# Performance work log

Measured on AMD Instinct MI355X. Metric: run time of the kernel, lower is better.

## Reference

```python
import jax, jax.numpy as jnp
import numpy as np

V, S, D, H, L, F = 32000, 1024, 1024, 16, 6, 4096
DH = D // H          # 64
HALF = DH // 2       # 32
EPS = 1e-5
ROPE_BASE = 10000.0


def setup_inputs() -> dict:
    key = jax.random.key(0)
    ks = jax.random.split(key, 16)
    std = 0.02
    inp = {
        "tokens": jax.random.randint(ks[0], (4, S), 0, V),
        "tok_emb": jax.random.normal(ks[1], (V, D), jnp.float32) * std,
        "ln1_s": jnp.ones((L, D), jnp.float32),
        "ln1_b": jnp.zeros((L, D), jnp.float32),
        "w_qkv": jax.random.normal(ks[2], (L, D, 3 * D), jnp.float32) * std,
        "w_proj": jax.random.normal(ks[3], (L, D, D), jnp.float32) * std,
        "ln2_s": jnp.ones((L, D), jnp.float32),
        "ln2_b": jnp.zeros((L, D), jnp.float32),
        "w_in": jax.random.normal(ks[4], (L, D, 2 * F), jnp.float32) * std,
        "w_out": jax.random.normal(ks[5], (L, F, D), jnp.float32) * std,
        "lnf_s": jnp.ones((D,), jnp.float32),
        "lnf_b": jnp.zeros((D,), jnp.float32),
        "w_score": jax.random.normal(ks[6], (D, 1), jnp.float32) * std,
        "w_cls": jax.random.normal(ks[7], (D, S), jnp.float32) * std,
    }
    return inp


def _layernorm(x, s, b):
    m = x.mean(-1, keepdims=True)
    v = ((x - m) ** 2).mean(-1, keepdims=True)
    return (x - m) * jax.lax.rsqrt(v + EPS) * s + b


def _rotate_half(x):
    x_even = x[..., ::2]
    x_odd = x[..., 1::2]
    return jnp.stack((-x_odd, x_even), axis=-1).reshape(x.shape)


def _rope_tables():
    inv_freq = 1.0 / (ROPE_BASE ** (jnp.arange(0, DH, 2, dtype=jnp.float32) / DH))
    pos = jnp.arange(S, dtype=jnp.float32)
    freqs = jnp.outer(pos, inv_freq)               # [S, DH/2]
    cos = jnp.repeat(jnp.cos(freqs), 2, axis=-1)   # [S, DH]
    sin = jnp.repeat(jnp.sin(freqs), 2, axis=-1)
    return cos, sin


def _forward(tokens, tok_emb, ln1_s, ln1_b, w_qkv, w_proj, ln2_s, ln2_b,
             w_in, w_out, lnf_s, lnf_b, w_score, w_cls):
    B = tokens.shape[0]
    cos, sin = _rope_tables()                      # [S, DH], broadcast over B,H
    lower = jnp.tril(jnp.ones((S, S), jnp.bool_))  # j <= i -> "down" subspace
    scale = HALF ** -0.5

    h = tok_emb[tokens]                            # [B, S, D]

    def block(h, p):
        l1s, l1b, Wqkv, Wp, l2s, l2b, Wi, Wo = p
        # --- dual-triangle attention ---
        qkv = _layernorm(h, l1s, l1b) @ Wqkv       # [B, S, 3D]
        q, k, v = jnp.split(qkv, 3, axis=-1)
        def heads(t):
            return t.reshape(B, S, H, DH).transpose(0, 2, 1, 3)  # [B,H,S,DH]
        q, k, v = heads(q), heads(k), heads(v)
        q = q * cos + _rotate_half(q) * sin
        k = k * cos + _rotate_half(k) * sin
        a_up = jnp.einsum('bhqd,bhkd->bhqk', q[..., :HALF], k[..., :HALF]) * scale
        a_dn = jnp.einsum('bhqd,bhkd->bhqk', q[..., HALF:], k[..., HALF:]) * scale
        logits = jnp.where(lower, a_dn, a_up)
        w = jax.nn.softmax(logits, axis=-1)
        o = jnp.einsum('bhqk,bhkd->bhqd', w, v)
        o = o.transpose(0, 2, 1, 3).reshape(B, S, D) @ Wp
        h = h + o
        # --- SwiGLU MLP ---
        g = _layernorm(h, l2s, l2b) @ Wi           # [B, S, 2F]
        a, b = jnp.split(g, 2, axis=-1)
        h = h + (jax.nn.silu(a) * b) @ Wo
        return h, None

    h, _ = jax.lax.scan(block, h, (ln1_s, ln1_b, w_qkv, w_proj, ln2_s, ln2_b, w_in, w_out))

    # pooling head: per-position scores -> softmax over positions -> weighted sum
    h = _layernorm(h, lnf_s, lnf_b)
    scores = h @ w_score                           # [B, S, 1]
    pw = jax.nn.softmax(scores, axis=1)
    pooled = jnp.sum(pw * h, axis=1)               # [B, D]
    return pooled @ w_cls                          # [B, S] logits over positions


def reference(tokens, tok_emb, ln1_s, ln1_b, w_qkv, w_proj, ln2_s, ln2_b,
              w_in, w_out, lnf_s, lnf_b, w_score, w_cls):
    return _forward(tokens, tok_emb, ln1_s, ln1_b, w_qkv, w_proj, ln2_s, ln2_b,
                    w_in, w_out, lnf_s, lnf_b, w_score, w_cls)
```

## Files before the change

### kernel.cpp

```cpp
#include <hip/hip_runtime.h>

#define Bsz 4
#define Ssz 1024
#define Dsz 1024
#define Hn  16
#define DHn 64
#define Ln  6
#define Fsz 4096
#define SCALE_ 0.1767766952966369f

typedef unsigned long long u64;
typedef __attribute__((ext_vector_type(8))) short bf16x8;
typedef __attribute__((ext_vector_type(4))) float f32x4;

__device__ __forceinline__ unsigned short f2bf(float f) {
  union { float f; unsigned int u; } v; v.f = f;
  unsigned int u = v.u + 0x7fffu + ((v.u >> 16) & 1u);
  return (unsigned short)(u >> 16);
}
__device__ __forceinline__ float bf2f(unsigned short h) {
  union { unsigned int u; float f; } v; v.u = ((unsigned int)h) << 16;
  return v.f;
}
__device__ __forceinline__ void gload_lds16(const void* g, void* lds) {
  __builtin_amdgcn_global_load_lds(
      (const __attribute__((address_space(1))) unsigned int*)g,
      (__attribute__((address_space(3))) unsigned int*)lds, 16, 0, 0);
}

__device__ __forceinline__ int swz_addr(int r, int lq) {
  int line = r >> 1;
  int u = ((r & 1) << 2) | lq;
  int s = u ^ (line & 7);
  return line * 128 + s * 16;
}

__global__ __launch_bounds__(256) void k_cossin(float* __restrict__ cosT, float* __restrict__ sinT) {
  int idx = blockIdx.x * 256 + threadIdx.x;
  if (idx >= Ssz * 32) return;
  int s = idx >> 5, i = idx & 31;
  float inv = powf(10000.f, -((float)(2 * i)) / 64.f);
  float f = (float)s * inv;
  cosT[idx] = cosf(f);
  sinT[idx] = sinf(f);
}

__global__ __launch_bounds__(256) void k_embed(const int* __restrict__ tokens,
                                               const float* __restrict__ emb,
                                               float* __restrict__ h) {
  int rs = blockIdx.x;
  int t = threadIdx.x;
  int tok = tokens[rs];
  *(float4*)&h[(u64)rs * Dsz + t * 4] = *(const float4*)&emb[(u64)tok * Dsz + t * 4];
}

template <int BF16OUT>
__global__ __launch_bounds__(256) void k_layernorm(const float* __restrict__ x,
                                                   const float* __restrict__ sc,
                                                   const float* __restrict__ bi,
                                                   void* outv) {
  int row = blockIdx.x, t = threadIdx.x;
  const float* xr = x + (u64)row * Dsz;
  float4 v = *(const float4*)&xr[t * 4];
  float sm = v.x + v.y + v.z + v.w;
  float sq = v.x * v.x + v.y * v.y + v.z * v.z + v.w * v.w;
#pragma unroll
  for (int m = 1; m < 64; m <<= 1) { sm += __shfl_xor(sm, m); sq += __shfl_xor(sq, m); }
  __shared__ float r1[4], r2[4];
  if ((t & 63) == 0) { r1[t >> 6] = sm; r2[t >> 6] = sq; }
  __syncthreads();
  sm = r1[0] + r1[1] + r1[2] + r1[3];
  sq = r2[0] + r2[1] + r2[2] + r2[3];
  float mean = sm * (1.f / Dsz);
  float inv = rsqrtf(sq * (1.f / Dsz) - mean * mean + 1e-5f);
  float4 s4 = *(const float4*)&sc[t * 4];
  float4 b4 = *(const float4*)&bi[t * 4];
  float y0 = (v.x - mean) * inv * s4.x + b4.x;
  float y1 = (v.y - mean) * inv * s4.y + b4.y;
  float y2 = (v.z - mean) * inv * s4.z + b4.z;
  float y3 = (v.w - mean) * inv * s4.w + b4.w;
  if (BF16OUT) {
    ushort4 o; o.x = f2bf(y0); o.y = f2bf(y1); o.z = f2bf(y2); o.w = f2bf(y3);
    *(ushort4*)((unsigned short*)outv + (u64)row * Dsz + t * 4) = o;
  } else {
    float4 o; o.x = y0; o.y = y1; o.z = y2; o.w = y3;
    *(float4*)((float*)outv + (u64)row * Dsz + t * 4) = o;
  }
}

__global__ __launch_bounds__(256) void k_wt(const float* __restrict__ in,
                                            unsigned short* __restrict__ out, int K, int N) {
  in += (u64)blockIdx.z * K * N;
  out += (u64)blockIdx.z * K * N;
  __shared__ float tile[32][33];
  int nb = blockIdx.x * 32, kb = blockIdx.y * 32;
  int t = threadIdx.x;
  int r = t >> 3, c4 = (t & 7) * 4;
  float4 v = *(const float4*)&in[(u64)(kb + r) * N + nb + c4];
  tile[r][c4] = v.x; tile[r][c4 + 1] = v.y; tile[r][c4 + 2] = v.z; tile[r][c4 + 3] = v.w;
  __syncthreads();
  ushort4 o;
  o.x = f2bf(tile[c4][r]); o.y = f2bf(tile[c4 + 1][r]);
  o.z = f2bf(tile[c4 + 2][r]); o.w = f2bf(tile[c4 + 3][r]);
  *(ushort4*)&out[(u64)(nb + r) * K + kb + c4] = o;
}

__global__ __launch_bounds__(256) void k_wt_pair(const float* __restrict__ in,
                                                 unsigned short* __restrict__ out) {
  in += (u64)blockIdx.z * Dsz * 2 * Fsz;
  out += (u64)blockIdx.z * 2 * Fsz * Dsz;
  __shared__ float tile[32][33];
  int nb = blockIdx.x * 32, kb = blockIdx.y * 32;
  int t = threadIdx.x;
  int r = t >> 3, c4 = (t & 7) * 4;
  int s0 = nb >> 1;
  int srccol = (c4 < 16) ? (s0 + c4) : (Fsz + s0 + (c4 - 16));
  float4 v = *(const float4*)&in[(u64)(kb + r) * (2 * Fsz) + srccol];
  tile[r][c4] = v.x; tile[r][c4 + 1] = v.y; tile[r][c4 + 2] = v.z; tile[r][c4 + 3] = v.w;
  __syncthreads();
  int sc = (r >> 1) + (r & 1) * 16;
  ushort4 o;
  o.x = f2bf(tile[c4][sc]); o.y = f2bf(tile[c4 + 1][sc]);
  o.z = f2bf(tile[c4 + 2][sc]); o.w = f2bf(tile[c4 + 3][sc]);
  *(ushort4*)&out[(u64)(nb + r) * Dsz + kb + c4] = o;
}

template <int EPI>
__global__ __launch_bounds__(256, 2) void k_ring128(const unsigned short* __restrict__ A,
                                                    const unsigned short* __restrict__ Bt,
                                                    const float* resid, void* Cout,
                                                    int M, int N, int K) {
  __shared__ char lds[4][16384] __attribute__((aligned(16)));
  int t = threadIdx.x, w = t >> 6, l = t & 63;
  int wm = w >> 1, wn = w & 1;
  int lr = l & 15, lq = l >> 4;
  int bn = blockIdx.x, bm = blockIdx.y;
  int NT = K >> 5;
  int g0 = t, g1 = t + 256;
  int L0 = g0 >> 3, u0 = (g0 & 7) ^ (L0 & 7), row0 = 2 * L0 + (u0 >> 2), kc0 = (u0 & 3) * 8;
  int L1 = g1 >> 3, u1 = (g1 & 7) ^ (L1 & 7), row1 = 2 * L1 + (u1 >> 2), kc1 = (u1 & 3) * 8;
  const char* Asrc0 = (const char*)(A + (u64)(bm * 128 + row0) * K + kc0);
  const char* Asrc1 = (const char*)(A + (u64)(bm * 128 + row1) * K + kc1);
  const char* Bsrc0 = (const char*)(Bt + (u64)(bn * 128 + row0) * K + kc0);
  const char* Bsrc1 = (const char*)(Bt + (u64)(bn * 128 + row1) * K + kc1);
  f32x4 acc[4][4];
#pragma unroll
  for (int i = 0; i < 4; ++i)
#pragma unroll
    for (int j = 0; j < 4; ++j) acc[i][j] = (f32x4){0.f, 0.f, 0.f, 0.f};
#define STG128(jj) { char* d_ = lds[(jj) & 3]; \
    gload_lds16(Asrc0 + (u64)(jj) * 64, d_ + g0 * 16); \
    gload_lds16(Asrc1 + (u64)(jj) * 64, d_ + g1 * 16); \
    gload_lds16(Bsrc0 + (u64)(jj) * 64, d_ + 8192 + g0 * 16); \
    gload_lds16(Bsrc1 + (u64)(jj) * 64, d_ + 8192 + g1 * 16); }
  STG128(0); STG128(1); STG128(2);
  for (int j = 0; j < NT; ++j) {
    if (j < NT - 2)       asm volatile("s_waitcnt vmcnt(8)" ::: "memory");
    else if (j == NT - 2) asm volatile("s_waitcnt vmcnt(4)" ::: "memory");
    else                  asm volatile("s_waitcnt vmcnt(0)" ::: "memory");
    __builtin_amdgcn_s_barrier();
    __builtin_amdgcn_sched_barrier(0);
    const char* Ab = lds[j & 3];
    const char* Bb = lds[j & 3] + 8192;
    if (j + 3 < NT) STG128(j + 3);
    bf16x8 afrag[4], bfrag[4];
#pragma unroll
    for (int ni = 0; ni < 4; ++ni)
      bfrag[ni] = *(const bf16x8*)(Bb + swz_addr(wn * 64 + ni * 16 + lr, lq));
#pragma unroll
    for (int mi = 0; mi < 4; ++mi)
      afrag[mi] = *(const bf16x8*)(Ab + swz_addr(wm * 64 + mi * 16 + lr, lq));
    __builtin_amdgcn_s_setprio(1);
#pragma unroll
    for (int mi = 0; mi < 4; ++mi)
#pragma unroll
      for (int ni = 0; ni < 4; ++ni)
        acc[mi][ni] = __builtin_amdgcn_mfma_f32_16x16x32_bf16(afrag[mi], bfrag[ni], acc[mi][ni], 0, 0, 0);
    __builtin_amdgcn_s_setprio(0);
  }
#undef STG128
#pragma unroll
  for (int mi = 0; mi < 4; ++mi)
#pragma unroll
    for (int ni = 0; ni < 4; ++ni)
#pragma unroll
      for (int r = 0; r < 4; ++r) {
        int row = bm * 128 + wm * 64 + mi * 16 + lq * 4 + r;
        int col = bn * 128 + wn * 64 + ni * 16 + lr;
        float v = acc[mi][ni][r];
        if (EPI == 3) {
          float pv = __shfl_xor(v, 1);
          if ((lr & 1) == 0) {
            float res = v / (1.f + __expf(-v)) * pv;
            ((unsigned short*)Cout)[(u64)row * (N >> 1) + (col >> 1)] = f2bf(res);
          }
        } else {
          u64 idx = (u64)row * N + col;
          if (EPI == 1) ((unsigned short*)Cout)[idx] = f2bf(v);
          else ((float*)Cout)[idx] = resid[idx] + v;
        }
      }
}

__global__ __launch_bounds__(256) void k_rope_heads(const unsigned short* __restrict__ qkv,
                                                    const float* __restrict__ cosT,
                                                    const float* __restrict__ sinT,
                                                    unsigned short* __restrict__ q_r,
                                                    unsigned short* __restrict__ k_r,
                                                    unsigned short* __restrict__ v_t) {
  int st = blockIdx.x, hh = blockIdx.y, b = blockIdx.z;
  int t = threadIdx.x;
  int r = t >> 2, cg = (t & 3) * 16;
  int s = st * 64 + r;
  u64 rowb = ((u64)(b * Ssz + s)) * (3 * Dsz);
  u64 bh = (u64)(b * Hn + hh);
  const unsigned int* qp = (const unsigned int*)(qkv + rowb + hh * 64 + cg);
  const unsigned int* kp = (const unsigned int*)(qkv + rowb + Dsz + hh * 64 + cg);
  const unsigned short* vp = qkv + rowb + 2 * Dsz + hh * 64 + cg;
  uint4 qv0 = *(const uint4*)qp, qv1 = *(const uint4*)(qp + 4);
  uint4 kv0 = *(const uint4*)kp, kv1 = *(const uint4*)(kp + 4);
  int i0 = s * 32 + (cg >> 1);
  float4 cA0 = *(const float4*)&cosT[i0], cA1 = *(const float4*)&cosT[i0 + 4];
  float4 sA0 = *(const float4*)&sinT[i0], sA1 = *(const float4*)&sinT[i0 + 4];
  unsigned int qw[8] = {qv0.x, qv0.y, qv0.z, qv0.w, qv1.x, qv1.y, qv1.z, qv1.w};
  unsigned int kw[8] = {kv0.x, kv0.y, kv0.z, kv0.w, kv1.x, kv1.y, kv1.z, kv1.w};
  float cA[8] = {cA0.x, cA0.y, cA0.z, cA0.w, cA1.x, cA1.y, cA1.z, cA1.w};
  float sA[8] = {sA0.x, sA0.y, sA0.z, sA0.w, sA1.x, sA1.y, sA1.z, sA1.w};
  unsigned int oq[8], ok[8];
#pragma unroll
  for (int j = 0; j < 8; ++j) {
    float c = cA[j], sn = sA[j];
    float qe = bf2f((unsigned short)(qw[j] & 0xffff)), qo = bf2f((unsigned short)(qw[j] >> 16));
    float ke = bf2f((unsigned short)(kw[j] & 0xffff)), ko = bf2f((unsigned short)(kw[j] >> 16));
    oq[j] = (unsigned int)f2bf(qe * c - qo * sn) | ((unsigned int)f2bf(qo * c + qe * sn) << 16);
    ok[j] = (unsigned int)f2bf(ke * c - ko * sn) | ((unsigned int)f2bf(ko * c + ke * sn) << 16);
  }
  u64 dst = (bh * Ssz + s) * 64 + cg;
  uint4 a0; a0.x = oq[0]; a0.y = oq[1]; a0.z = oq[2]; a0.w = oq[3];
  uint4 a1; a1.x = oq[4]; a1.y = oq[5]; a1.z = oq[6]; a1.w = oq[7];
  ((uint4*)&q_r[dst])[0] = a0; ((uint4*)&q_r[dst])[1] = a1;
  uint4 b0; b0.x = ok[0]; b0.y = ok[1]; b0.z = ok[2]; b0.w = ok[3];
  uint4 b1; b1.x = ok[4]; b1.y = ok[5]; b1.z = ok[6]; b1.w = ok[7];
  ((uint4*)&k_r[dst])[0] = b0; ((uint4*)&k_r[dst])[1] = b1;
  __shared__ unsigned short vt_lds[64][65];
  uint4 vv0 = *(const uint4*)vp, vv1 = *(const uint4*)(vp + 8);
  unsigned int vw[8] = {vv0.x, vv0.y, vv0.z, vv0.w, vv1.x, vv1.y, vv1.z, vv1.w};
#pragma unroll
  for (int j = 0; j < 8; ++j) {
    vt_lds[r][cg + 2 * j] = (unsigned short)(vw[j] & 0xffff);
    vt_lds[r][cg + 2 * j + 1] = (unsigned short)(vw[j] >> 16);
  }
  __syncthreads();
  unsigned int ov[8];
#pragma unroll
  for (int j = 0; j < 8; ++j) {
    unsigned short lo = vt_lds[cg + 2 * j][r], hi = vt_lds[cg + 2 * j + 1][r];
    ov[j] = (unsigned int)lo | ((unsigned int)hi << 16);
  }
  u64 vdst = bh * ((u64)DHn * Ssz) + (u64)r * Ssz + st * 64 + cg;
  uint4 c0v; c0v.x = ov[0]; c0v.y = ov[1]; c0v.z = ov[2]; c0v.w = ov[3];
  uint4 c1v; c1v.x = ov[4]; c1v.y = ov[5]; c1v.z = ov[6]; c1v.w = ov[7];
  ((uint4*)&v_t[vdst])[0] = c0v; ((uint4*)&v_t[vdst])[1] = c1v;
}

__global__ __launch_bounds__(256) void k_attn(const unsigned short* __restrict__ qr,
                                              const unsigned short* __restrict__ kr,
                                              const unsigned short* __restrict__ vt,
                                              unsigned short* __restrict__ outp) {
  __shared__ unsigned short Klds[2][2][64 * 32] __attribute__((aligned(16)));
  __shared__ unsigned short Vlds[2][2][64 * 32] __attribute__((aligned(16)));
  __shared__ unsigned short Plds[4][16 * 64] __attribute__((aligned(16)));
  int qt = blockIdx.x, hh = blockIdx.y, b = blockIdx.z;
  int t = threadIdx.x, w = t >> 6, l = t & 63;
  int lr = l & 15, lq = l >> 4;
  u64 bh = (u64)(b * Hn + hh);
  const unsigned short* Qp = qr + bh * (Ssz * DHn);
  const unsigned short* Kp = kr + bh * (Ssz * DHn);
  const unsigned short* Vp = vt + bh * ((u64)DHn * Ssz);
  int q0 = qt * 64 + w * 16;
  bf16x8 qlo = *(const bf16x8*)&Qp[(q0 + lr) * DHn + lq * 8];
  bf16x8 qhi = *(const bf16x8*)&Qp[(q0 + lr) * DHn + 32 + lq * 8];
  int srow = t >> 2;
  int scol8 = (t & 3) * 8;
#define STAGEKV(bufi, kbase)                                                         \
  do {                                                                               \
    gload_lds16(&Kp[((kbase) + srow) * 64 + scol8],      (char*)&Klds[bufi][0][0] + t * 16); \
    gload_lds16(&Kp[((kbase) + srow) * 64 + 32 + scol8], (char*)&Klds[bufi][1][0] + t * 16); \
    gload_lds16(&Vp[(u64)srow * Ssz + (kbase) + scol8],      (char*)&Vlds[bufi][0][0] + t * 16); \
    gload_lds16(&Vp[(u64)srow * Ssz + (kbase) + 32 + scol8], (char*)&Vlds[bufi][1][0] + t * 16); \
  } while (0)
  float m_col = -1e30f, lsum = 0.f;
  float m_row[4] = {-1e30f, -1e30f, -1e30f, -1e30f};
  f32x4 o[4];
#pragma unroll
  for (int r = 0; r < 4; ++r) o[r] = (f32x4){0.f, 0.f, 0.f, 0.f};
  char* Pw = (char*)&Plds[w][0];

  STAGEKV(0, 0);
  asm volatile("s_waitcnt vmcnt(0)" ::: "memory");
  __syncthreads();
  int buf = 0;
  for (int kb = 0; kb < Ssz; kb += 64) {
    if (kb + 64 < Ssz) STAGEKV(buf ^ 1, kb + 64);
    float p[4][4];
#pragma unroll
    for (int ct = 0; ct < 4; ++ct) {
      bf16x8 klo = *(const bf16x8*)&Klds[buf][0][(ct * 16 + lr) * 32 + lq * 8];
      bf16x8 khi = *(const bf16x8*)&Klds[buf][1][(ct * 16 + lr) * 32 + lq * 8];
      f32x4 z = (f32x4){0.f, 0.f, 0.f, 0.f};
      f32x4 slo = __builtin_amdgcn_mfma_f32_16x16x32_bf16(klo, qlo, z, 0, 0, 0);
      f32x4 shi = __builtin_amdgcn_mfma_f32_16x16x32_bf16(khi, qhi, z, 0, 0, 0);
      int kg0 = kb + ct * 16 + lq * 4;
      int qg = q0 + lr;
#pragma unroll
      for (int r = 0; r < 4; ++r) p[ct][r] = (kg0 + r <= qg ? shi[r] : slo[r]) * SCALE_;
    }
    float tm = p[0][0];
#pragma unroll
    for (int ct = 0; ct < 4; ++ct)
#pragma unroll
      for (int r = 0; r < 4; ++r) tm = fmaxf(tm, p[ct][r]);
    tm = fmaxf(tm, __shfl_xor(tm, 16));
    tm = fmaxf(tm, __shfl_xor(tm, 32));
    float m_new = fmaxf(m_col, tm);
    lsum *= __expf(m_col - m_new);
    m_col = m_new;
#pragma unroll
    for (int r = 0; r < 4; ++r) {
      float mr = __shfl(m_col, lq * 4 + r);
      float scf = __expf(m_row[r] - mr);
      m_row[r] = mr;
      o[0][r] *= scf; o[1][r] *= scf; o[2][r] *= scf; o[3][r] *= scf;
    }
#pragma unroll
    for (int ct = 0; ct < 4; ++ct) {
      float e0 = __expf(p[ct][0] - m_col);
      float e1 = __expf(p[ct][1] - m_col);
      float e2 = __expf(p[ct][2] - m_col);
      float e3 = __expf(p[ct][3] - m_col);
      lsum += e0 + e1 + e2 + e3;
      ushort4 pk; pk.x = f2bf(e0); pk.y = f2bf(e1); pk.z = f2bf(e2); pk.w = f2bf(e3);
      int byte_ = (lr * 128 + ct * 32 + lq * 8) ^ ((lr & 7) << 4);
      *(ushort4*)(Pw + byte_) = pk;
    }
    asm volatile("s_waitcnt lgkmcnt(0)" ::: "memory");
    __builtin_amdgcn_sched_barrier(0);
#pragma unroll
    for (int ks = 0; ks < 2; ++ks) {
      int pb = (lr * 128 + ks * 64 + lq * 16) ^ ((lr & 7) << 4);
      bf16x8 pa = *(const bf16x8*)(Pw + pb);
#pragma unroll
      for (int nt = 0; nt < 4; ++nt) {
        bf16x8 vb = *(const bf16x8*)&Vlds[buf][ks][(nt * 16 + lr) * 32 + lq * 8];
        o[nt] = __builtin_amdgcn_mfma_f32_16x16x32_bf16(pa, vb, o[nt], 0, 0, 0);
      }
    }
    asm volatile("s_waitcnt vmcnt(0)" ::: "memory");
    __syncthreads();
    buf ^= 1;
  }
  lsum += __shfl_xor(lsum, 16);
  lsum += __shfl_xor(lsum, 32);
  u64 obase = ((u64)b * Ssz) * Dsz + (u64)hh * DHn;
#pragma unroll
  for (int r = 0; r < 4; ++r) {
    float ls = __shfl(lsum, lq * 4 + r);
    float inv = 1.f / ls;
    int qrow = q0 + lq * 4 + r;
#pragma unroll
    for (int nt = 0; nt < 4; ++nt)
      outp[obase + (u64)qrow * Dsz + nt * 16 + lr] = f2bf(o[nt][r] * inv);
  }
#undef STAGEKV
}

__global__ __launch_bounds__(256) void k_scores(const float* __restrict__ hf,
                                                const float* __restrict__ wsc,
                                                float* __restrict__ scores) {
  int row = blockIdx.x * 4 + (threadIdx.x >> 6);
  int l = threadIdx.x & 63;
  const float* xr = hf + (u64)row * Dsz;
  float acc = 0.f;
#pragma unroll
  for (int j = 0; j < 4; ++j) {
    float4 v = *(const float4*)&xr[(j * 64 + l) * 4];
    float4 ww = *(const float4*)&wsc[(j * 64 + l) * 4];
    acc += v.x * ww.x + v.y * ww.y + v.z * ww.z + v.w * ww.w;
  }
#pragma unroll
  for (int m = 1; m < 64; m <<= 1) acc += __shfl_xor(acc, m);
  if (l == 0) scores[row] = acc;
}

__global__ __launch_bounds__(256) void k_softmax_s(const float* __restrict__ sc,
                                                   float* __restrict__ pw) {
  int b = blockIdx.x, t = threadIdx.x;
  const float* sr = sc + b * Ssz;
  float4 v = *(const float4*)&sr[t * 4];
  float mx = fmaxf(fmaxf(v.x, v.y), fmaxf(v.z, v.w));
#pragma unroll
  for (int m = 1; m < 64; m <<= 1) mx = fmaxf(mx, __shfl_xor(mx, m));
  __shared__ float red[4];
  if ((t & 63) == 0) red[t >> 6] = mx;
  __syncthreads();
  mx = fmaxf(fmaxf(red[0], red[1]), fmaxf(red[2], red[3]));
  float e0 = __expf(v.x - mx), e1 = __expf(v.y - mx), e2 = __expf(v.z - mx), e3 = __expf(v.w - mx);
  float sm = e0 + e1 + e2 + e3;
#pragma unroll
  for (int m = 1; m < 64; m <<= 1) sm += __shfl_xor(sm, m);
  __shared__ float red2[4];
  if ((t & 63) == 0) red2[t >> 6] = sm;
  __syncthreads();
  sm = red2[0] + red2[1] + red2[2] + red2[3];
  float inv = 1.f / sm;
  float4 o; o.x = e0 * inv; o.y = e1 * inv; o.z = e2 * inv; o.w = e3 * inv;
  *(float4*)&pw[b * Ssz + t * 4] = o;
}

__global__ __launch_bounds__(256) void k_pool1(const float* __restrict__ hf,
                                               const float* __restrict__ pw,
                                               float* __restrict__ part) {
  int d = blockIdx.x * 256 + threadIdx.x;
  int b = blockIdx.y, scn = blockIdx.z;
  const float* pwb = pw + b * Ssz + scn * 64;
  const float* hb = hf + ((u64)(b * Ssz + scn * 64)) * Dsz + d;
  float acc = 0.f;
#pragma unroll 4
  for (int s = 0; s < 64; ++s) acc += pwb[s] * hb[(u64)s * Dsz];
  part[(u64)(b * 16 + scn) * Dsz + d] = acc;
}
__global__ __launch_bounds__(256) void k_pool2(const float* __restrict__ part,
                                               float* __restrict__ pooled) {
  int d = blockIdx.x * 256 + threadIdx.x;
  int b = blockIdx.y;
  float acc = 0.f;
#pragma unroll
  for (int i = 0; i < 16; ++i) acc += part[(u64)(b * 16 + i) * Dsz + d];
  pooled[b * Dsz + d] = acc;
}

__global__ __launch_bounds__(256) void k_cls1(const float* __restrict__ pooled,
                                              const float* __restrict__ wcls,
                                              float* __restrict__ part) {
  int n = blockIdx.x * 64 + (threadIdx.x & 63);
  int b = threadIdx.x >> 6;
  int kz = blockIdx.y;
  const float* pb = pooled + b * Dsz + kz * 128;
  const float* wb = wcls + (u64)(kz * 128) * Ssz + n;
  float acc = 0.f;
#pragma unroll 4
  for (int k = 0; k < 128; ++k) acc += pb[k] * wb[(u64)k * Ssz];
  part[(u64)(kz * 4 + b) * Ssz + n] = acc;
}
__global__ __launch_bounds__(256) void k_cls2(const float* __restrict__ part,
                                              float* __restrict__ outp) {
  int n = blockIdx.x * 64 + (threadIdx.x & 63);
  int b = threadIdx.x >> 6;
  float acc = 0.f;
#pragma unroll
  for (int kz = 0; kz < 8; ++kz) acc += part[(u64)(kz * 4 + b) * Ssz + n];
  outp[b * Ssz + n] = acc;
}

extern "C" void kernel_launch(void* const* d_in, const int* in_sizes, int n_in,
                              void* d_out, int out_size, void* d_ws, size_t ws_size,
                              hipStream_t stream) {
  (void)in_sizes; (void)n_in; (void)out_size; (void)ws_size;
  const int*   tokens  = (const int*)  d_in[0];
  const float* tok_emb = (const float*)d_in[1];
  const float* ln1_s   = (const float*)d_in[2];
  const float* ln1_b   = (const float*)d_in[3];
  const float* w_qkv   = (const float*)d_in[4];
  const float* w_proj  = (const float*)d_in[5];
  const float* ln2_s   = (const float*)d_in[6];
  const float* ln2_b   = (const float*)d_in[7];
  const float* w_in    = (const float*)d_in[8];
  const float* w_out   = (const float*)d_in[9];
  const float* lnf_s   = (const float*)d_in[10];
  const float* lnf_b   = (const float*)d_in[11];
  const float* w_score = (const float*)d_in[12];
  const float* w_cls   = (const float*)d_in[13];
  float* outp = (float*)d_out;
  char* ws = (char*)d_ws;

  unsigned short* qkv    = (unsigned short*)(ws + 0);
  unsigned short* q_r    = (unsigned short*)(ws + 25165824ull);
  unsigned short* k_r    = (unsigned short*)(ws + 33554432ull);
  unsigned short* v_t    = (unsigned short*)(ws + 41943040ull);
  unsigned short* a_out  = (unsigned short*)(ws + 50331648ull);
  float*          hf     = (float*)(ws + 0);
  unsigned short* x_ln   = (unsigned short*)(ws + 67108864ull);
  unsigned short* mbuf   = (unsigned short*)(ws + 75497472ull);
  float*          h      = (float*)(ws + 109051904ull);
  float* cosT    = (float*)(ws + 125829120ull);
  float* sinT    = (float*)(ws + 125960192ull);
  float* scoresb = (float*)(ws + 126091264ull);
  float* pwb     = (float*)(ws + 126107648ull);
  float* pooledb = (float*)(ws + 126124032ull);
  float* poolpart= (float*)(ws + 126140416ull);
  float* clspart = (float*)(ws + 126402560ull);
  unsigned short* wqkv_t = (unsigned short*)(ws + 134217728ull);
  unsigned short* wproj_t= (unsigned short*)(ws + 171966464ull);
  unsigned short* win_t  = (unsigned short*)(ws + 184549376ull);
  unsigned short* wout_t = (unsigned short*)(ws + 285212672ull);

  dim3 blk(256);
  k_cossin<<<dim3(128), blk, 0, stream>>>(cosT, sinT);
  k_embed<<<dim3(4096), blk, 0, stream>>>(tokens, tok_emb, h);
  k_wt<<<dim3(96, 32, 6), blk, 0, stream>>>(w_qkv, wqkv_t, Dsz, 3 * Dsz);
  k_wt<<<dim3(32, 32, 6), blk, 0, stream>>>(w_proj, wproj_t, Dsz, Dsz);
  k_wt_pair<<<dim3(256, 32, 6), blk, 0, stream>>>(w_in, win_t);
  k_wt<<<dim3(32, 128, 6), blk, 0, stream>>>(w_out, wout_t, Fsz, Dsz);

  for (int l = 0; l < Ln; ++l) {
    unsigned short* wq = wqkv_t + (u64)l * 3145728ull;
    unsigned short* wp = wproj_t + (u64)l * 1048576ull;
    unsigned short* wi = win_t + (u64)l * 8388608ull;
    unsigned short* wo = wout_t + (u64)l * 4194304ull;
    k_layernorm<1><<<dim3(4096), blk, 0, stream>>>(h, ln1_s + l * Dsz, ln1_b + l * Dsz, (void*)x_ln);
    k_ring128<1><<<dim3(24, 32), blk, 0, stream>>>(x_ln, wq, nullptr, (void*)qkv, 4096, 3072, 1024);
    k_rope_heads<<<dim3(16, 16, 4), blk, 0, stream>>>(qkv, cosT, sinT, q_r, k_r, v_t);
    k_attn<<<dim3(16, 16, 4), blk, 0, stream>>>(q_r, k_r, v_t, a_out);
    k_ring128<2><<<dim3(8, 32), blk, 0, stream>>>(a_out, wp, h, (void*)h, 4096, 1024, 1024);
    k_layernorm<1><<<dim3(4096), blk, 0, stream>>>(h, ln2_s + l * Dsz, ln2_b + l * Dsz, (void*)x_ln);
    k_ring128<3><<<dim3(64, 32), blk, 0, stream>>>(x_ln, wi, nullptr, (void*)mbuf, 4096, 8192, 1024);
    k_ring128<2><<<dim3(8, 32), blk, 0, stream>>>(mbuf, wo, h, (void*)h, 4096, 1024, 4096);
  }

  k_layernorm<0><<<dim3(4096), blk, 0, stream>>>(h, lnf_s, lnf_b, (void*)hf);
  k_scores<<<dim3(1024), blk, 0, stream>>>(hf, w_score, scoresb);
  k_softmax_s<<<dim3(4), blk, 0, stream>>>(scoresb, pwb);
  k_pool1<<<dim3(4, 4, 16), blk, 0, stream>>>(hf, pwb, poolpart);
  k_pool2<<<dim3(4, 4), blk, 0, stream>>>(poolpart, pooledb);
  k_cls1<<<dim3(16, 8), blk, 0, stream>>>(pooledb, w_cls, clspart);
  k_cls2<<<dim3(16), blk, 0, stream>>>(clspart, outp);
}
```

Measured before the change: 2.000 ms.

## Use 128x64 GEMM tiles for narrow GEMMs and exp2-based lazy rescaling in attention

The GEMM kernel is templated on tile width, and the QKV, projection and MLP-out GEMMs now run with 128x64 tiles. This doubles the block count for the N=1024 GEMMs to fill more compute units and allows three blocks per CU. The attention softmax folds log2(e) into the scale so it can use exp2f. It also skips the running max/output rescale when no lane's tile max exceeds the current max. The trade-off is less operand reuse per tile and an extra wave-wide vote per iteration.

```diff
diff --git a/kernel.cpp b/kernel.cpp
--- a/kernel.cpp
+++ b/kernel.cpp
@@ -8,6 +8,7 @@
 #define Ln  6
 #define Fsz 4096
 #define SCALE_ 0.1767766952966369f
+#define LOG2E_ 1.4426950408889634f
 
 typedef unsigned long long u64;
 typedef __attribute__((ext_vector_type(8))) short bf16x8;
@@ -125,12 +126,16 @@
   *(ushort4*)&out[(u64)(nb + r) * Dsz + kb + c4] = o;
 }
 
-template <int EPI>
-__global__ __launch_bounds__(256, 2) void k_ring128(const unsigned short* __restrict__ A,
-                                                    const unsigned short* __restrict__ Bt,
-                                                    const float* resid, void* Cout,
-                                                    int M, int N, int K) {
-  __shared__ char lds[4][16384] __attribute__((aligned(16)));
+template <int BN, int EPI>
+__global__ __launch_bounds__(256, (BN == 128) ? 2 : 3)
+void k_ring(const unsigned short* __restrict__ A,
+            const unsigned short* __restrict__ Bt,
+            const float* resid, void* Cout,
+            int M, int N, int K) {
+  constexpr int RING = (128 + BN) * 64;
+  constexpr int WN = BN / 2;
+  constexpr int NF = WN / 16;
+  __shared__ char lds[4][RING] __attribute__((aligned(16)));
   int t = threadIdx.x, w = t >> 6, l = t & 63;
   int wm = w >> 1, wn = w & 1;
   int lr = l & 15, lq = l >> 4;
@@ -141,32 +146,38 @@
   int L1 = g1 >> 3, u1 = (g1 & 7) ^ (L1 & 7), row1 = 2 * L1 + (u1 >> 2), kc1 = (u1 & 3) * 8;
   const char* Asrc0 = (const char*)(A + (u64)(bm * 128 + row0) * K + kc0);
   const char* Asrc1 = (const char*)(A + (u64)(bm * 128 + row1) * K + kc1);
-  const char* Bsrc0 = (const char*)(Bt + (u64)(bn * 128 + row0) * K + kc0);
-  const char* Bsrc1 = (const char*)(Bt + (u64)(bn * 128 + row1) * K + kc1);
-  f32x4 acc[4][4];
+  const char* Bsrc0 = (const char*)(Bt + (u64)(bn * BN + row0) * K + kc0);
+  const char* Bsrc1 = (const char*)(Bt + (u64)(bn * BN + ((BN == 128) ? row1 : row0)) * K + kc1);
+  f32x4 acc[4][NF];
 #pragma unroll
   for (int i = 0; i < 4; ++i)
 #pragma unroll
-    for (int j = 0; j < 4; ++j) acc[i][j] = (f32x4){0.f, 0.f, 0.f, 0.f};
-#define STG128(jj) { char* d_ = lds[(jj) & 3]; \
+    for (int j = 0; j < NF; ++j) acc[i][j] = (f32x4){0.f, 0.f, 0.f, 0.f};
+#define STG(jj) { char* d_ = lds[(jj) & 3]; \
     gload_lds16(Asrc0 + (u64)(jj) * 64, d_ + g0 * 16); \
     gload_lds16(Asrc1 + (u64)(jj) * 64, d_ + g1 * 16); \
     gload_lds16(Bsrc0 + (u64)(jj) * 64, d_ + 8192 + g0 * 16); \
-    gload_lds16(Bsrc1 + (u64)(jj) * 64, d_ + 8192 + g1 * 16); }
-  STG128(0); STG128(1); STG128(2);
+    if constexpr (BN == 128) gload_lds16(Bsrc1 + (u64)(jj) * 64, d_ + 8192 + g1 * 16); }
+  STG(0); STG(1); STG(2);
   for (int j = 0; j < NT; ++j) {
-    if (j < NT - 2)       asm volatile("s_waitcnt vmcnt(8)" ::: "memory");
-    else if (j == NT - 2) asm volatile("s_waitcnt vmcnt(4)" ::: "memory");
-    else                  asm volatile("s_waitcnt vmcnt(0)" ::: "memory");
+    if constexpr (BN == 128) {
+      if (j < NT - 2)       asm volatile("s_waitcnt vmcnt(8)" ::: "memory");
+      else if (j == NT - 2) asm volatile("s_waitcnt vmcnt(4)" ::: "memory");
+      else                  asm volatile("s_waitcnt vmcnt(0)" ::: "memory");
+    } else {
+      if (j < NT - 2)       asm volatile("s_waitcnt vmcnt(6)" ::: "memory");
+      else if (j == NT - 2) asm volatile("s_waitcnt vmcnt(3)" ::: "memory");
+      else                  asm volatile("s_waitcnt vmcnt(0)" ::: "memory");
+    }
     __builtin_amdgcn_s_barrier();
     __builtin_amdgcn_sched_barrier(0);
     const char* Ab = lds[j & 3];
     const char* Bb = lds[j & 3] + 8192;
-    if (j + 3 < NT) STG128(j + 3);
-    bf16x8 afrag[4], bfrag[4];
-#pragma unroll
-    for (int ni = 0; ni < 4; ++ni)
-      bfrag[ni] = *(const bf16x8*)(Bb + swz_addr(wn * 64 + ni * 16 + lr, lq));
+    if (j + 3 < NT) STG(j + 3);
+    bf16x8 afrag[4], bfrag[NF];
+#pragma unroll
+    for (int ni = 0; ni < NF; ++ni)
+      bfrag[ni] = *(const bf16x8*)(Bb + swz_addr(wn * WN + ni * 16 + lr, lq));
 #pragma unroll
     for (int mi = 0; mi < 4; ++mi)
       afrag[mi] = *(const bf16x8*)(Ab + swz_addr(wm * 64 + mi * 16 + lr, lq));
@@ -174,19 +185,19 @@
 #pragma unroll
     for (int mi = 0; mi < 4; ++mi)
 #pragma unroll
-      for (int ni = 0; ni < 4; ++ni)
+      for (int ni = 0; ni < NF; ++ni)
         acc[mi][ni] = __builtin_amdgcn_mfma_f32_16x16x32_bf16(afrag[mi], bfrag[ni], acc[mi][ni], 0, 0, 0);
     __builtin_amdgcn_s_setprio(0);
   }
-#undef STG128
+#undef STG
 #pragma unroll
   for (int mi = 0; mi < 4; ++mi)
 #pragma unroll
-    for (int ni = 0; ni < 4; ++ni)
+    for (int ni = 0; ni < NF; ++ni)
 #pragma unroll
       for (int r = 0; r < 4; ++r) {
         int row = bm * 128 + wm * 64 + mi * 16 + lq * 4 + r;
-        int col = bn * 128 + wn * 64 + ni * 16 + lr;
+        int col = bn * BN + wn * WN + ni * 16 + lr;
         float v = acc[mi][ni][r];
         if (EPI == 3) {
           float pv = __shfl_xor(v, 1);
@@ -300,6 +311,7 @@
   asm volatile("s_waitcnt vmcnt(0)" ::: "memory");
   __syncthreads();
   int buf = 0;
+  const float lsc = SCALE_ * LOG2E_;
   for (int kb = 0; kb < Ssz; kb += 64) {
     if (kb + 64 < Ssz) STAGEKV(buf ^ 1, kb + 64);
     float p[4][4];
@@ -313,7 +325,7 @@
       int kg0 = kb + ct * 16 + lq * 4;
       int qg = q0 + lr;
 #pragma unroll
-      for (int r = 0; r < 4; ++r) p[ct][r] = (kg0 + r <= qg ? shi[r] : slo[r]) * SCALE_;
+      for (int r = 0; r < 4; ++r) p[ct][r] = (kg0 + r <= qg ? shi[r] : slo[r]) * lsc;
     }
     float tm = p[0][0];
 #pragma unroll
@@ -322,22 +334,24 @@
       for (int r = 0; r < 4; ++r) tm = fmaxf(tm, p[ct][r]);
     tm = fmaxf(tm, __shfl_xor(tm, 16));
     tm = fmaxf(tm, __shfl_xor(tm, 32));
-    float m_new = fmaxf(m_col, tm);
-    lsum *= __expf(m_col - m_new);
-    m_col = m_new;
-#pragma unroll
-    for (int r = 0; r < 4; ++r) {
-      float mr = __shfl(m_col, lq * 4 + r);
-      float scf = __expf(m_row[r] - mr);
-      m_row[r] = mr;
-      o[0][r] *= scf; o[1][r] *= scf; o[2][r] *= scf; o[3][r] *= scf;
+    if (__any(tm > m_col)) {
+      float m_new = fmaxf(m_col, tm);
+      lsum *= exp2f(m_col - m_new);
+      m_col = m_new;
+#pragma unroll
+      for (int r = 0; r < 4; ++r) {
+        float mr = __shfl(m_col, lq * 4 + r);
+        float scf = exp2f(m_row[r] - mr);
+        m_row[r] = mr;
+        o[0][r] *= scf; o[1][r] *= scf; o[2][r] *= scf; o[3][r] *= scf;
+      }
     }
 #pragma unroll
     for (int ct = 0; ct < 4; ++ct) {
-      float e0 = __expf(p[ct][0] - m_col);
-      float e1 = __expf(p[ct][1] - m_col);
-      float e2 = __expf(p[ct][2] - m_col);
-      float e3 = __expf(p[ct][3] - m_col);
+      float e0 = exp2f(p[ct][0] - m_col);
+      float e1 = exp2f(p[ct][1] - m_col);
+      float e2 = exp2f(p[ct][2] - m_col);
+      float e3 = exp2f(p[ct][3] - m_col);
       lsum += e0 + e1 + e2 + e3;
       ushort4 pk; pk.x = f2bf(e0); pk.y = f2bf(e1); pk.z = f2bf(e2); pk.w = f2bf(e3);
       int byte_ = (lr * 128 + ct * 32 + lq * 8) ^ ((lr & 7) << 4);
@@ -518,13 +532,13 @@
     unsigned short* wi = win_t + (u64)l * 8388608ull;
     unsigned short* wo = wout_t + (u64)l * 4194304ull;
     k_layernorm<1><<<dim3(4096), blk, 0, stream>>>(h, ln1_s + l * Dsz, ln1_b + l * Dsz, (void*)x_ln);
-    k_ring128<1><<<dim3(24, 32), blk, 0, stream>>>(x_ln, wq, nullptr, (void*)qkv, 4096, 3072, 1024);
+    k_ring<64, 1><<<dim3(48, 32), blk, 0, stream>>>(x_ln, wq, nullptr, (void*)qkv, 4096, 3072, 1024);
     k_rope_heads<<<dim3(16, 16, 4), blk, 0, stream>>>(qkv, cosT, sinT, q_r, k_r, v_t);
     k_attn<<<dim3(16, 16, 4), blk, 0, stream>>>(q_r, k_r, v_t, a_out);
-    k_ring128<2><<<dim3(8, 32), blk, 0, stream>>>(a_out, wp, h, (void*)h, 4096, 1024, 1024);
+    k_ring<64, 2><<<dim3(16, 32), blk, 0, stream>>>(a_out, wp, h, (void*)h, 4096, 1024, 1024);
     k_layernorm<1><<<dim3(4096), blk, 0, stream>>>(h, ln2_s + l * Dsz, ln2_b + l * Dsz, (void*)x_ln);
-    k_ring128<3><<<dim3(64, 32), blk, 0, stream>>>(x_ln, wi, nullptr, (void*)mbuf, 4096, 8192, 1024);
-    k_ring128<2><<<dim3(8, 32), blk, 0, stream>>>(mbuf, wo, h, (void*)h, 4096, 1024, 4096);
+    k_ring<128, 3><<<dim3(64, 32), blk, 0, stream>>>(x_ln, wi, nullptr, (void*)mbuf, 4096, 8192, 1024);
+    k_ring<64, 2><<<dim3(16, 32), blk, 0, stream>>>(mbuf, wo, h, (void*)h, 4096, 1024, 4096);
   }
 
   k_layernorm<0><<<dim3(4096), blk, 0, stream>>>(h, lnf_s, lnf_b, (void*)hf);
```

Result: slower. 2.051 ms (+2.5%).

## Shrink GEMM ring to 3 stages, split-K the MLP down-projection, use exp2 softmax

Applied to the files above, without the earlier changes.

The GEMM kernel's LDS ring drops from four stages to three and launch bounds rise to three blocks per CU, trading prefetch depth for occupancy. The MLP down-projection now splits K in two across blockIdx.z, writing fp32 partials that a new kernel sums into the residual. This gives a 256-block launch more parallelism at the cost of extra partial-buffer traffic. The attention kernel folds log2e into the score scale, switches to exp2f, and skips rescaling when no lane's running max grows.

```diff
diff --git a/kernel.cpp b/kernel.cpp
--- a/kernel.cpp
+++ b/kernel.cpp
@@ -8,6 +8,7 @@
 #define Ln  6
 #define Fsz 4096
 #define SCALE_ 0.1767766952966369f
+#define LOG2E_ 1.4426950408889634f
 
 typedef unsigned long long u64;
 typedef __attribute__((ext_vector_type(8))) short bf16x8;
@@ -126,43 +127,46 @@
 }
 
 template <int EPI>
-__global__ __launch_bounds__(256, 2) void k_ring128(const unsigned short* __restrict__ A,
-                                                    const unsigned short* __restrict__ Bt,
-                                                    const float* resid, void* Cout,
-                                                    int M, int N, int K) {
-  __shared__ char lds[4][16384] __attribute__((aligned(16)));
+__global__ __launch_bounds__(256, 3)
+void k_ring(const unsigned short* __restrict__ A,
+            const unsigned short* __restrict__ Bt,
+            const float* resid, void* Cout,
+            int M, int N, int K, int KH) {
+  __shared__ char lds[3][16384] __attribute__((aligned(16)));
   int t = threadIdx.x, w = t >> 6, l = t & 63;
   int wm = w >> 1, wn = w & 1;
   int lr = l & 15, lq = l >> 4;
-  int bn = blockIdx.x, bm = blockIdx.y;
-  int NT = K >> 5;
+  int bn = blockIdx.x, bm = blockIdx.y, kz = blockIdx.z;
+  int NT = KH >> 5;
   int g0 = t, g1 = t + 256;
   int L0 = g0 >> 3, u0 = (g0 & 7) ^ (L0 & 7), row0 = 2 * L0 + (u0 >> 2), kc0 = (u0 & 3) * 8;
   int L1 = g1 >> 3, u1 = (g1 & 7) ^ (L1 & 7), row1 = 2 * L1 + (u1 >> 2), kc1 = (u1 & 3) * 8;
-  const char* Asrc0 = (const char*)(A + (u64)(bm * 128 + row0) * K + kc0);
-  const char* Asrc1 = (const char*)(A + (u64)(bm * 128 + row1) * K + kc1);
-  const char* Bsrc0 = (const char*)(Bt + (u64)(bn * 128 + row0) * K + kc0);
-  const char* Bsrc1 = (const char*)(Bt + (u64)(bn * 128 + row1) * K + kc1);
+  const unsigned short* Az = A + (u64)kz * KH;
+  const unsigned short* Bz = Bt + (u64)kz * KH;
+  const char* Asrc0 = (const char*)(Az + (u64)(bm * 128 + row0) * K + kc0);
+  const char* Asrc1 = (const char*)(Az + (u64)(bm * 128 + row1) * K + kc1);
+  const char* Bsrc0 = (const char*)(Bz + (u64)(bn * 128 + row0) * K + kc0);
+  const char* Bsrc1 = (const char*)(Bz + (u64)(bn * 128 + row1) * K + kc1);
   f32x4 acc[4][4];
 #pragma unroll
   for (int i = 0; i < 4; ++i)
 #pragma unroll
     for (int j = 0; j < 4; ++j) acc[i][j] = (f32x4){0.f, 0.f, 0.f, 0.f};
-#define STG128(jj) { char* d_ = lds[(jj) & 3]; \
+#define STG(slot, jj) { char* d_ = lds[slot]; \
     gload_lds16(Asrc0 + (u64)(jj) * 64, d_ + g0 * 16); \
     gload_lds16(Asrc1 + (u64)(jj) * 64, d_ + g1 * 16); \
     gload_lds16(Bsrc0 + (u64)(jj) * 64, d_ + 8192 + g0 * 16); \
     gload_lds16(Bsrc1 + (u64)(jj) * 64, d_ + 8192 + g1 * 16); }
-  STG128(0); STG128(1); STG128(2);
+  STG(0, 0); STG(1, 1);
+  int cs = 0, ss = 2;
   for (int j = 0; j < NT; ++j) {
-    if (j < NT - 2)       asm volatile("s_waitcnt vmcnt(8)" ::: "memory");
-    else if (j == NT - 2) asm volatile("s_waitcnt vmcnt(4)" ::: "memory");
-    else                  asm volatile("s_waitcnt vmcnt(0)" ::: "memory");
+    if (j < NT - 1) asm volatile("s_waitcnt vmcnt(4)" ::: "memory");
+    else            asm volatile("s_waitcnt vmcnt(0)" ::: "memory");
     __builtin_amdgcn_s_barrier();
     __builtin_amdgcn_sched_barrier(0);
-    const char* Ab = lds[j & 3];
-    const char* Bb = lds[j & 3] + 8192;
-    if (j + 3 < NT) STG128(j + 3);
+    const char* Ab = lds[cs];
+    const char* Bb = lds[cs] + 8192;
+    if (j + 2 < NT) STG(ss, j + 2);
     bf16x8 afrag[4], bfrag[4];
 #pragma unroll
     for (int ni = 0; ni < 4; ++ni)
@@ -177,8 +181,11 @@
       for (int ni = 0; ni < 4; ++ni)
         acc[mi][ni] = __builtin_amdgcn_mfma_f32_16x16x32_bf16(afrag[mi], bfrag[ni], acc[mi][ni], 0, 0, 0);
     __builtin_amdgcn_s_setprio(0);
-  }
-#undef STG128
+    cs = (cs == 2) ? 0 : cs + 1;
+    ss = (ss == 2) ? 0 : ss + 1;
+  }
+#undef STG
+  u64 zoff = (u64)kz * M * N;
 #pragma unroll
   for (int mi = 0; mi < 4; ++mi)
 #pragma unroll
@@ -196,10 +203,22 @@
           }
         } else {
           u64 idx = (u64)row * N + col;
-          if (EPI == 1) ((unsigned short*)Cout)[idx] = f2bf(v);
+          if (EPI == 0) ((float*)Cout)[zoff + idx] = v;
+          else if (EPI == 1) ((unsigned short*)Cout)[idx] = f2bf(v);
           else ((float*)Cout)[idx] = resid[idx] + v;
         }
       }
+}
+
+__global__ __launch_bounds__(256) void k_redres(const float* __restrict__ p0,
+                                                const float* __restrict__ p1,
+                                                float* __restrict__ h) {
+  u64 i = ((u64)blockIdx.x * 256 + threadIdx.x) * 4;
+  float4 a = *(float4*)&h[i];
+  float4 b = *(const float4*)&p0[i];
+  float4 c = *(const float4*)&p1[i];
+  a.x += b.x + c.x; a.y += b.y + c.y; a.z += b.z + c.z; a.w += b.w + c.w;
+  *(float4*)&h[i] = a;
 }
 
 __global__ __launch_bounds__(256) void k_rope_heads(const unsigned short* __restrict__ qkv,
@@ -300,6 +319,7 @@
   asm volatile("s_waitcnt vmcnt(0)" ::: "memory");
   __syncthreads();
   int buf = 0;
+  const float lsc = SCALE_ * LOG2E_;
   for (int kb = 0; kb < Ssz; kb += 64) {
     if (kb + 64 < Ssz) STAGEKV(buf ^ 1, kb + 64);
     float p[4][4];
@@ -313,7 +333,7 @@
       int kg0 = kb + ct * 16 + lq * 4;
       int qg = q0 + lr;
 #pragma unroll
-      for (int r = 0; r < 4; ++r) p[ct][r] = (kg0 + r <= qg ? shi[r] : slo[r]) * SCALE_;
+      for (int r = 0; r < 4; ++r) p[ct][r] = (kg0 + r <= qg ? shi[r] : slo[r]) * lsc;
     }
     float tm = p[0][0];
 #pragma unroll
@@ -322,22 +342,24 @@
       for (int r = 0; r < 4; ++r) tm = fmaxf(tm, p[ct][r]);
     tm = fmaxf(tm, __shfl_xor(tm, 16));
     tm = fmaxf(tm, __shfl_xor(tm, 32));
-    float m_new = fmaxf(m_col, tm);
-    lsum *= __expf(m_col - m_new);
-    m_col = m_new;
-#pragma unroll
-    for (int r = 0; r < 4; ++r) {
-      float mr = __shfl(m_col, lq * 4 + r);
-      float scf = __expf(m_row[r] - mr);
-      m_row[r] = mr;
-      o[0][r] *= scf; o[1][r] *= scf; o[2][r] *= scf; o[3][r] *= scf;
+    if (__any(tm > m_col)) {
+      float m_new = fmaxf(m_col, tm);
+      lsum *= exp2f(m_col - m_new);
+      m_col = m_new;
+#pragma unroll
+      for (int r = 0; r < 4; ++r) {
+        float mr = __shfl(m_col, lq * 4 + r);
+        float scf = exp2f(m_row[r] - mr);
+        m_row[r] = mr;
+        o[0][r] *= scf; o[1][r] *= scf; o[2][r] *= scf; o[3][r] *= scf;
+      }
     }
 #pragma unroll
     for (int ct = 0; ct < 4; ++ct) {
-      float e0 = __expf(p[ct][0] - m_col);
-      float e1 = __expf(p[ct][1] - m_col);
-      float e2 = __expf(p[ct][2] - m_col);
-      float e3 = __expf(p[ct][3] - m_col);
+      float e0 = exp2f(p[ct][0] - m_col);
+      float e1 = exp2f(p[ct][1] - m_col);
+      float e2 = exp2f(p[ct][2] - m_col);
+      float e3 = exp2f(p[ct][3] - m_col);
       lsum += e0 + e1 + e2 + e3;
       ushort4 pk; pk.x = f2bf(e0); pk.y = f2bf(e1); pk.z = f2bf(e2); pk.w = f2bf(e3);
       int byte_ = (lr * 128 + ct * 32 + lq * 8) ^ ((lr & 7) << 4);
@@ -503,6 +525,7 @@
   unsigned short* wproj_t= (unsigned short*)(ws + 171966464ull);
   unsigned short* win_t  = (unsigned short*)(ws + 184549376ull);
   unsigned short* wout_t = (unsigned short*)(ws + 285212672ull);
+  float* skpart  = (float*)(ws + 335544320ull);
 
   dim3 blk(256);
   k_cossin<<<dim3(128), blk, 0, stream>>>(cosT, sinT);
@@ -518,13 +541,14 @@
     unsigned short* wi = win_t + (u64)l * 8388608ull;
     unsigned short* wo = wout_t + (u64)l * 4194304ull;
     k_layernorm<1><<<dim3(4096), blk, 0, stream>>>(h, ln1_s + l * Dsz, ln1_b + l * Dsz, (void*)x_ln);
-    k_ring128<1><<<dim3(24, 32), blk, 0, stream>>>(x_ln, wq, nullptr, (void*)qkv, 4096, 3072, 1024);
+    k_ring<1><<<dim3(24, 32), blk, 0, stream>>>(x_ln, wq, nullptr, (void*)qkv, 4096, 3072, 1024, 1024);
     k_rope_heads<<<dim3(16, 16, 4), blk, 0, stream>>>(qkv, cosT, sinT, q_r, k_r, v_t);
     k_attn<<<dim3(16, 16, 4), blk, 0, stream>>>(q_r, k_r, v_t, a_out);
-    k_ring128<2><<<dim3(8, 32), blk, 0, stream>>>(a_out, wp, h, (void*)h, 4096, 1024, 1024);
+    k_ring<2><<<dim3(8, 32), blk, 0, stream>>>(a_out, wp, h, (void*)h, 4096, 1024, 1024, 1024);
     k_layernorm<1><<<dim3(4096), blk, 0, stream>>>(h, ln2_s + l * Dsz, ln2_b + l * Dsz, (void*)x_ln);
-    k_ring128<3><<<dim3(64, 32), blk, 0, stream>>>(x_ln, wi, nullptr, (void*)mbuf, 4096, 8192, 1024);
-    k_ring128<2><<<dim3(8, 32), blk, 0, stream>>>(mbuf, wo, h, (void*)h, 4096, 1024, 4096);
+    k_ring<3><<<dim3(64, 32), blk, 0, stream>>>(x_ln, wi, nullptr, (void*)mbuf, 4096, 8192, 1024, 1024);
+    k_ring<0><<<dim3(8, 32, 2), blk, 0, stream>>>(mbuf, wo, nullptr, (void*)skpart, 4096, 1024, 4096, 2048);
+    k_redres<<<dim3(4096), blk, 0, stream>>>(skpart, skpart + 4194304ull, h);
   }
 
   k_layernorm<0><<<dim3(4096), blk, 0, stream>>>(h, lnf_s, lnf_b, (void*)hf);
```

Result: no change. 1.970 ms (-1.5%).
